# Performance work log

Hardware: AMD Instinct MI355X
Metric: run time of the kernel (lower is better)

## Reference

```python
import jax, jax.numpy as jnp
import numpy as np

B, N, D, H = 4, 512, 512, 8
DK = D // H
DIM_G = 64            # trignometric_embedding=True
WAVE_LEN = 1000.0


def box_relational_embedding(f_g):
    # f_g: [B, N, 4] = (x_min, x_max, y_min, y_max)
    x_min, x_max, y_min, y_max = jnp.split(f_g, 4, axis=-1)   # each [B, N, 1]
    cx = (x_min + x_max) * 0.5
    cy = (y_min + y_max) * 0.5
    w = x_max - x_min + 1.0
    h = y_max - y_min + 1.0
    # pairwise deltas: [B, N, 1] - [B, 1, N] -> [B, N, N]
    dx = jnp.log(jnp.clip(jnp.abs((cx - jnp.swapaxes(cx, 1, 2)) / w), 1e-3, None))
    dy = jnp.log(jnp.clip(jnp.abs((cy - jnp.swapaxes(cy, 1, 2)) / h), 1e-3, None))
    dw = jnp.log(w / jnp.swapaxes(w, 1, 2))
    dh = jnp.log(h / jnp.swapaxes(h, 1, 2))
    pos = jnp.stack([dx, dy, dw, dh], axis=-1)                # [B, N, N, 4]
    n_freq = DIM_G // 8                                       # 8
    feat_range = jnp.arange(n_freq, dtype=pos.dtype) / n_freq
    dim_mat = 1.0 / (WAVE_LEN ** feat_range)                  # [8]
    mul = (100.0 * pos)[..., None] * dim_mat                  # [B, N, N, 4, 8]
    mul = mul.reshape(B, N, N, 4 * n_freq)                    # [B, N, N, 32]
    return jnp.concatenate([jnp.sin(mul), jnp.cos(mul)], axis=-1)  # [B, N, N, 64]


def setup_inputs() -> dict:
    key = jax.random.key(0)
    ks = jax.random.split(key, 12)
    s = 0.02
    return {
        "input_query": jax.random.normal(ks[0], (B, N, D), jnp.float32),
        "input_key": jax.random.normal(ks[1], (B, N, D), jnp.float32),
        "input_value": jax.random.normal(ks[2], (B, N, D), jnp.float32),
        "input_box": jax.random.uniform(ks[3], (B, N, 4), jnp.float32),
        "mask": jnp.ones((B, N, N), jnp.int32),
        # 4 d_model->d_model linears (q, k, v, out); stored as [in, out]
        "Wq": jax.random.normal(ks[4], (D, D), jnp.float32) * s,
        "bq": jnp.zeros((D,), jnp.float32),
        "Wk": jax.random.normal(ks[5], (D, D), jnp.float32) * s,
        "bk": jnp.zeros((D,), jnp.float32),
        "Wv": jax.random.normal(ks[6], (D, D), jnp.float32) * s,
        "bv": jnp.zeros((D,), jnp.float32),
        "Wo": jax.random.normal(ks[7], (D, D), jnp.float32) * s,
        "bo": jnp.zeros((D,), jnp.float32),
        # the 8 per-head WGs (dim_g -> 1) stacked into a single [dim_g, H] matrix
        "Wg": jax.random.normal(ks[8], (DIM_G, H), jnp.float32) * s,
        "bg": jnp.zeros((H,), jnp.float32),
    }


def reference(input_query, input_key, input_value, input_box, mask,
              Wq, bq, Wk, bk, Wv, bv, Wo, bo, Wg, bg):
    # geometry embeddings -> per-head geometric weights
    geo_emb = box_relational_embedding(input_box)                 # [B, N, N, 64]
    geo_w = jax.nn.relu(jnp.einsum("bijg,gh->bhij", geo_emb, Wg)
                        + bg[None, :, None, None])                # [B, H, N, N]

    # q/k/v projections split into heads
    q = (input_query @ Wq + bq).reshape(B, N, H, DK)
    k = (input_key @ Wk + bk).reshape(B, N, H, DK)
    v = (input_value @ Wv + bv).reshape(B, N, H, DK)

    scores = jnp.einsum("bqhd,bkhd->bhqk", q, k) / np.sqrt(DK)    # [B, H, N, N]
    scores = jnp.where(mask[:, None, :, :] == 0, -1e9, scores)

    logits = jnp.log(jnp.clip(geo_w, 1e-6, None)) + scores
    attn = jax.nn.softmax(logits, axis=-1)                        # [B, H, N, N]

    out = jnp.einsum("bhqk,bkhd->bqhd", attn, v).reshape(B, N, D)
    return out @ Wo + bo                                          # [B, N, D]
```

## Files before the change

kernel.cpp:

```cpp
#include <hip/hip_runtime.h>
#include <hip/hip_bf16.h>

#define Bq 4
#define Nn 512
#define Dd 512
#define Hh 8
#define DKk 64

typedef __bf16 bf16x8 __attribute__((ext_vector_type(8)));
typedef float f32x4 __attribute__((ext_vector_type(4)));
typedef unsigned short u16x8 __attribute__((ext_vector_type(8)));

static __device__ __forceinline__ unsigned short f2bf(float f) {
    unsigned int u = __float_as_uint(f);
    return (unsigned short)((u + 0x7FFFu + ((u >> 16) & 1u)) >> 16);
}
static __device__ __forceinline__ unsigned short f2h(float f) {
    union { _Float16 h; unsigned short u; } cv;
    cv.h = (_Float16)f;
    return cv.u;
}
static __device__ __forceinline__ float h2f(unsigned short us) {
    union { _Float16 h; unsigned short u; } cv;
    cv.u = us;
    return (float)cv.h;
}

struct PreArgs {
    const float* A[3];
    const float* W[3];
    const float* bias[3];
    unsigned short* C[3];
    int ns[3], cs[3];
    float scale[3];
    const float* box;
    const int* mask;
    const float* Wg;
    const float* bg;
    unsigned short* lw;
};

__global__ __launch_bounds__(256) void pre_k(PreArgs pa)
{
    __shared__ __align__(16) char pool[10496];
    const int t = threadIdx.x;
    const int r_ = (int)(blockIdx.x % 19), g_ = (int)(blockIdx.x / 19);

    if (r_ < 16) {
        float (*WgS)[8] = (float(*)[8])pool;
        float* bgS = (float*)(pool + 2048);
        if (t < 128) ((float4*)&WgS[0][0])[t] = ((const float4*)pa.Wg)[t];
        if (t < 8) bgS[t] = pa.bg[t];
        __syncthreads();

        const int gb = g_ * 16 + r_;
        const size_t gid = (size_t)gb * 256 + t;
        const int j = (int)(gid & (Nn - 1));
        const int i = (int)((gid >> 9) & (Nn - 1));
        const int b = (int)(gid >> 18);

        const float4 bi = *(const float4*)(pa.box + ((size_t)b * Nn + i) * 4);
        const float4 bj = *(const float4*)(pa.box + ((size_t)b * Nn + j) * 4);
        const float cxi = (bi.x + bi.y) * 0.5f, cyi = (bi.z + bi.w) * 0.5f;
        const float wi = bi.y - bi.x + 1.0f, hi = bi.w - bi.z + 1.0f;
        const float cxj = (bj.x + bj.y) * 0.5f, cyj = (bj.z + bj.w) * 0.5f;
        const float wj = bj.y - bj.x + 1.0f, hj = bj.w - bj.z + 1.0f;

        const float pos0 = __logf(fmaxf(fabsf((cxi - cxj) / wi), 1e-3f));
        const float pos1 = __logf(fmaxf(fabsf((cyi - cyj) / hi), 1e-3f));
        const float pos2 = __logf(wi / wj);
        const float pos3 = __logf(hi / hj);

        const float dimr[8] = {1.0f, 0.421696503f, 0.177827941f, 0.0749894209f,
                               0.0316227766f, 0.0133352143f, 0.00562341325f, 0.00237137371f};

        float acc[8] = {0.f, 0.f, 0.f, 0.f, 0.f, 0.f, 0.f, 0.f};
#pragma unroll 1
        for (int p = 0; p < 4; ++p) {
            const float base = 100.0f * ((p == 0) ? pos0 : (p == 1) ? pos1 : (p == 2) ? pos2 : pos3);
            const int g0 = p << 3;
#pragma unroll
            for (int f = 0; f < 8; ++f) {
                float s, c;
                __sincosf(base * dimr[f], &s, &c);
                const int g = g0 + f;
                const float4 wa = *(const float4*)&WgS[g][0];
                const float4 wb = *(const float4*)&WgS[g][4];
                const float4 ca = *(const float4*)&WgS[g + 32][0];
                const float4 cb = *(const float4*)&WgS[g + 32][4];
                acc[0] = fmaf(s, wa.x, fmaf(c, ca.x, acc[0]));
                acc[1] = fmaf(s, wa.y, fmaf(c, ca.y, acc[1]));
                acc[2] = fmaf(s, wa.z, fmaf(c, ca.z, acc[2]));
                acc[3] = fmaf(s, wa.w, fmaf(c, ca.w, acc[3]));
                acc[4] = fmaf(s, wb.x, fmaf(c, cb.x, acc[4]));
                acc[5] = fmaf(s, wb.y, fmaf(c, cb.y, acc[5]));
                acc[6] = fmaf(s, wb.z, fmaf(c, cb.z, acc[6]));
                acc[7] = fmaf(s, wb.w, fmaf(c, cb.w, acc[7]));
            }
        }

        const int mk = pa.mask[gid];
        const size_t ob_ = (size_t)b * Hh * Nn * Nn + (size_t)i * Nn + j;
#pragma unroll
        for (int hh = 0; hh < 8; ++hh) {
            const float gw = acc[hh] + bgS[hh];
            const float lwv = (mk == 0) ? -60000.0f : __logf(fmaxf(gw, 1e-6f));
            pa.lw[ob_ + (size_t)hh * Nn * Nn] = f2h(lwv);
        }
    } else {
        unsigned short (*Alds)[40] = (unsigned short(*)[40])pool;
        unsigned short (*Blds)[40] = (unsigned short(*)[40])(pool + 5120);
        const int qid = g_ * 3 + (r_ - 16);
        const int z = qid % 3, tid = qid / 3;
        const int col0 = (tid & 7) << 6, row0 = (tid >> 3) << 6;
        const float* __restrict__ A = pa.A[z];
        const float* __restrict__ W = pa.W[z];

        const int l = t & 63, wq = t >> 6;
        const int lr = t >> 2, lc8 = (t & 3) << 3;
        const int bn = t & 63, bk8 = (t >> 6) << 3;
        const int lrow = l & 15, lgrp = l >> 4;

        f32x4 acc[4];
#pragma unroll
        for (int nf = 0; nf < 4; ++nf) acc[nf] = (f32x4){0.f, 0.f, 0.f, 0.f};

        for (int k0 = 0; k0 < Dd; k0 += 32) {
            const float* Ap = A + (size_t)(row0 + lr) * Dd + k0 + lc8;
            const float4 f1 = *(const float4*)Ap;
            const float4 f2 = *(const float4*)(Ap + 4);
            u16x8 a8;
            a8[0] = f2bf(f1.x); a8[1] = f2bf(f1.y); a8[2] = f2bf(f1.z); a8[3] = f2bf(f1.w);
            a8[4] = f2bf(f2.x); a8[5] = f2bf(f2.y); a8[6] = f2bf(f2.z); a8[7] = f2bf(f2.w);
            u16x8 b8;
#pragma unroll
            for (int jj = 0; jj < 8; ++jj)
                b8[jj] = f2bf(W[(size_t)(k0 + bk8 + jj) * Dd + col0 + bn]);
            __syncthreads();
            *(u16x8*)&Alds[lr][lc8] = a8;
            *(u16x8*)&Blds[bn][bk8] = b8;
            __syncthreads();
            const bf16x8 a = *(const bf16x8*)&Alds[wq * 16 + lrow][lgrp << 3];
#pragma unroll
            for (int nf = 0; nf < 4; ++nf) {
                const bf16x8 bfr = *(const bf16x8*)&Blds[nf * 16 + lrow][lgrp << 3];
                acc[nf] = __builtin_amdgcn_mfma_f32_16x16x32_bf16(a, bfr, acc[nf], 0, 0, 0);
            }
        }

        const float* bias = pa.bias[z];
        const float scl = pa.scale[z];
        const int ns = pa.ns[z], cs = pa.cs[z];
        const int rbase = row0 + wq * 16 + (lgrp << 2);
#pragma unroll
        for (int nf = 0; nf < 4; ++nf) {
            const int colg = col0 + nf * 16 + lrow;
            const float bv = bias[colg];
#pragma unroll
            for (int r = 0; r < 4; ++r) {
                const int rowg = rbase + r;
                const size_t addr = (size_t)(rowg >> 9) * ((size_t)Nn * Dd)
                                  + (size_t)(rowg & (Nn - 1)) * ns + (size_t)colg * cs;
                pa.C[z][addr] = f2bf((acc[nf][r] + bv) * scl);
            }
        }
    }
}

__global__ __launch_bounds__(256) void attn_k(
    const unsigned short* __restrict__ qb, const unsigned short* __restrict__ kb,
    const unsigned short* __restrict__ vt, const unsigned short* __restrict__ lwh,
    unsigned short* __restrict__ ob)
{
    __shared__ unsigned short Qlds[64][72];
    __shared__ unsigned short Klds[64][72];
    __shared__ unsigned short Vlds[64][72];
    __shared__ unsigned short Plds[4][16][72];
    __shared__ unsigned short LWs[64][72];

    const int t = threadIdx.x;
    const int l = t & 63, wq = t >> 6;
    const int bx = blockIdx.x;
    const int qt = bx & 7, h = (bx >> 3) & 7, b = bx >> 6;
    const int q0 = qt << 6;
    const int sr = t >> 3, sc8 = (t & 7) << 3;
    const int lrow = l & 15, lgrp = l >> 4;
    const int qr0 = t >> 3, c80 = (t & 7) << 3;
    const int qr1 = 32 + (t >> 3), c81 = c80;

    const size_t lwb = ((size_t)(b * Hh + h) * Nn + q0) * Nn;

#pragma unroll
    for (int it = 0; it < 2; ++it) {
        const int r = it * 32 + sr;
        *(u16x8*)&Qlds[r][sc8] =
            *(const u16x8*)(qb + (((size_t)b * Nn + q0 + r) * Hh + h) * DKk + sc8);
    }

    u16x8 kr[2], vr[2], lwr[2];
#pragma unroll
    for (int it = 0; it < 2; ++it) {
        const int r = it * 32 + sr;
        kr[it] = *(const u16x8*)(kb + (((size_t)b * Nn + r) * Hh + h) * DKk + sc8);
        vr[it] = *(const u16x8*)(vt + ((size_t)(b * Hh + h) * DKk + r) * Nn + sc8);
    }
    lwr[0] = *(const u16x8*)(lwh + lwb + (size_t)qr0 * Nn + c80);
    lwr[1] = *(const u16x8*)(lwh + lwb + (size_t)qr1 * Nn + c81);
#pragma unroll
    for (int it = 0; it < 2; ++it) {
        const int r = it * 32 + sr;
        *(u16x8*)&Klds[r][sc8] = kr[it];
        *(u16x8*)&Vlds[r][sc8] = vr[it];
    }
    *(u16x8*)&LWs[qr0][c80] = lwr[0];
    *(u16x8*)&LWs[qr1][c81] = lwr[1];
    __syncthreads();

    bf16x8 qa[2];
    qa[0] = *(const bf16x8*)&Qlds[wq * 16 + lrow][lgrp << 3];
    qa[1] = *(const bf16x8*)&Qlds[wq * 16 + lrow][32 + (lgrp << 3)];

    float m[4], lsum[4];
    f32x4 oacc[4];
#pragma unroll
    for (int r = 0; r < 4; ++r) { m[r] = -1e30f; lsum[r] = 0.f; }
#pragma unroll
    for (int fd = 0; fd < 4; ++fd) oacc[fd] = (f32x4){0.f, 0.f, 0.f, 0.f};

    for (int c = 0; c < 8; ++c) {
        if (c) __syncthreads();
        if (c < 7) {
            const int k1 = (c + 1) << 6;
#pragma unroll
            for (int it = 0; it < 2; ++it) {
                const int r = it * 32 + sr;
                kr[it] = *(const u16x8*)(kb + (((size_t)b * Nn + k1 + r) * Hh + h) * DKk + sc8);
                vr[it] = *(const u16x8*)(vt + ((size_t)(b * Hh + h) * DKk + r) * Nn + k1 + sc8);
            }
            lwr[0] = *(const u16x8*)(lwh + lwb + (size_t)qr0 * Nn + k1 + c80);
            lwr[1] = *(const u16x8*)(lwh + lwb + (size_t)qr1 * Nn + k1 + c81);
        }

        f32x4 sacc[4];
#pragma unroll
        for (int f = 0; f < 4; ++f) sacc[f] = (f32x4){0.f, 0.f, 0.f, 0.f};
#pragma unroll
        for (int ks = 0; ks < 2; ++ks)
#pragma unroll
            for (int f = 0; f < 4; ++f) {
                const bf16x8 kf = *(const bf16x8*)&Klds[f * 16 + lrow][(ks << 5) + (lgrp << 3)];
                sacc[f] = __builtin_amdgcn_mfma_f32_16x16x32_bf16(qa[ks], kf, sacc[f], 0, 0, 0);
            }

        float p[4][4], mx[4];
#pragma unroll
        for (int r = 0; r < 4; ++r) mx[r] = -1e30f;
#pragma unroll
        for (int f = 0; f < 4; ++f) {
#pragma unroll
            for (int r = 0; r < 4; ++r) {
                const float lg = sacc[f][r] + h2f(LWs[wq * 16 + lgrp * 4 + r][f * 16 + lrow]);
                p[f][r] = lg;
                mx[r] = fmaxf(mx[r], lg);
            }
        }
#pragma unroll
        for (int r = 0; r < 4; ++r) {
            float cm = mx[r];
            cm = fmaxf(cm, __shfl_xor(cm, 1));
            cm = fmaxf(cm, __shfl_xor(cm, 2));
            cm = fmaxf(cm, __shfl_xor(cm, 4));
            cm = fmaxf(cm, __shfl_xor(cm, 8));
            const float mn = fmaxf(m[r], cm);
            const float sc = __expf(m[r] - mn);
            m[r] = mn;
            float ps = 0.f;
#pragma unroll
            for (int f = 0; f < 4; ++f) {
                p[f][r] = __expf(p[f][r] - mn);
                ps += p[f][r];
            }
            ps += __shfl_xor(ps, 1);
            ps += __shfl_xor(ps, 2);
            ps += __shfl_xor(ps, 4);
            ps += __shfl_xor(ps, 8);
            lsum[r] = lsum[r] * sc + ps;
#pragma unroll
            for (int fd = 0; fd < 4; ++fd) oacc[fd][r] *= sc;
        }

#pragma unroll
        for (int f = 0; f < 4; ++f)
#pragma unroll
            for (int r = 0; r < 4; ++r)
                Plds[wq][lgrp * 4 + r][f * 16 + lrow] = f2bf(p[f][r]);

#pragma unroll
        for (int ks = 0; ks < 2; ++ks) {
            const bf16x8 pa = *(const bf16x8*)&Plds[wq][lrow][(ks << 5) + (lgrp << 3)];
#pragma unroll
            for (int fd = 0; fd < 4; ++fd) {
                const bf16x8 vf = *(const bf16x8*)&Vlds[fd * 16 + lrow][(ks << 5) + (lgrp << 3)];
                oacc[fd] = __builtin_amdgcn_mfma_f32_16x16x32_bf16(pa, vf, oacc[fd], 0, 0, 0);
            }
        }

        if (c < 7) {
            __syncthreads();
#pragma unroll
            for (int it = 0; it < 2; ++it) {
                const int r = it * 32 + sr;
                *(u16x8*)&Klds[r][sc8] = kr[it];
                *(u16x8*)&Vlds[r][sc8] = vr[it];
            }
            *(u16x8*)&LWs[qr0][c80] = lwr[0];
            *(u16x8*)&LWs[qr1][c81] = lwr[1];
        }
    }

#pragma unroll
    for (int r = 0; r < 4; ++r) {
        const float inv = 1.0f / lsum[r];
        const int qrow = q0 + wq * 16 + lgrp * 4 + r;
#pragma unroll
        for (int fd = 0; fd < 4; ++fd) {
            ob[(((size_t)b * Nn + qrow) * Hh + h) * DKk + fd * 16 + lrow] =
                f2bf(oacc[fd][r] * inv);
        }
    }
}

__global__ __launch_bounds__(256) void outproj_k(
    const unsigned short* __restrict__ A, const float* __restrict__ W,
    const float* __restrict__ bias, float* __restrict__ C)
{
    __shared__ unsigned short Alds[64][40];
    __shared__ unsigned short Blds[64][40];
    const int t = threadIdx.x;
    const int l = t & 63, wq = t >> 6;
    const int col0 = (int)(blockIdx.x) << 6, row0 = (int)(blockIdx.y) << 6;
    const int lr = t >> 2, lc8 = (t & 3) << 3;
    const int bn = t & 63, bk8 = (t >> 6) << 3;
    const int lrow = l & 15, lgrp = l >> 4;

    f32x4 acc[4];
#pragma unroll
    for (int nf = 0; nf < 4; ++nf) acc[nf] = (f32x4){0.f, 0.f, 0.f, 0.f};

    for (int k0 = 0; k0 < Dd; k0 += 32) {
        const u16x8 a8 = *(const u16x8*)(A + (size_t)(row0 + lr) * Dd + k0 + lc8);
        u16x8 b8;
#pragma unroll
        for (int jj = 0; jj < 8; ++jj)
            b8[jj] = f2bf(W[(size_t)(k0 + bk8 + jj) * Dd + col0 + bn]);
        __syncthreads();
        *(u16x8*)&Alds[lr][lc8] = a8;
        *(u16x8*)&Blds[bn][bk8] = b8;
        __syncthreads();
        const bf16x8 a = *(const bf16x8*)&Alds[wq * 16 + lrow][lgrp << 3];
#pragma unroll
        for (int nf = 0; nf < 4; ++nf) {
            const bf16x8 bfr = *(const bf16x8*)&Blds[nf * 16 + lrow][lgrp << 3];
            acc[nf] = __builtin_amdgcn_mfma_f32_16x16x32_bf16(a, bfr, acc[nf], 0, 0, 0);
        }
    }

    const int rbase = row0 + wq * 16 + (lgrp << 2);
#pragma unroll
    for (int nf = 0; nf < 4; ++nf) {
        const int colg = col0 + nf * 16 + lrow;
        const float bv = bias[colg];
#pragma unroll
        for (int r = 0; r < 4; ++r)
            C[(size_t)(rbase + r) * Dd + colg] = acc[nf][r] + bv;
    }
}

extern "C" void kernel_launch(void* const* d_in, const int* in_sizes, int n_in,
                              void* d_out, int out_size, void* d_ws, size_t ws_size,
                              hipStream_t stream)
{
    (void)in_sizes; (void)n_in; (void)out_size; (void)ws_size;

    const float* q_in = (const float*)d_in[0];
    const float* k_in = (const float*)d_in[1];
    const float* v_in = (const float*)d_in[2];
    const float* box  = (const float*)d_in[3];
    const int*   mask = (const int*)d_in[4];
    const float* Wq = (const float*)d_in[5];
    const float* bq = (const float*)d_in[6];
    const float* Wk = (const float*)d_in[7];
    const float* bk = (const float*)d_in[8];
    const float* Wv = (const float*)d_in[9];
    const float* bv = (const float*)d_in[10];
    const float* Wo = (const float*)d_in[11];
    const float* bo = (const float*)d_in[12];
    const float* Wg = (const float*)d_in[13];
    const float* bg = (const float*)d_in[14];
    float* out = (float*)d_out;

    char* ws = (char*)d_ws;
    unsigned short* qb  = (unsigned short*)(ws);
    unsigned short* kb  = (unsigned short*)(ws + (2u << 20));
    unsigned short* vt  = (unsigned short*)(ws + (4u << 20));
    unsigned short* ob  = (unsigned short*)(ws + (6u << 20));
    unsigned short* lwh = (unsigned short*)(ws + (8u << 20));

    PreArgs pa;
    pa.A[0] = q_in; pa.A[1] = k_in; pa.A[2] = v_in;
    pa.W[0] = Wq;   pa.W[1] = Wk;   pa.W[2] = Wv;
    pa.bias[0] = bq; pa.bias[1] = bk; pa.bias[2] = bv;
    pa.C[0] = qb; pa.C[1] = kb; pa.C[2] = vt;
    pa.ns[0] = Dd; pa.ns[1] = Dd; pa.ns[2] = 1;
    pa.cs[0] = 1;  pa.cs[1] = 1;  pa.cs[2] = Nn;
    pa.scale[0] = 0.125f; pa.scale[1] = 1.0f; pa.scale[2] = 1.0f;
    pa.box = box; pa.mask = mask; pa.Wg = Wg; pa.bg = bg; pa.lw = lwh;
    pre_k<<<dim3(4864), 256, 0, stream>>>(pa);

    attn_k<<<dim3(Bq * Hh * (Nn / 64)), 256, 0, stream>>>(qb, kb, vt, lwh, ob);

    outproj_k<<<dim3(8, 32), 256, 0, stream>>>(ob, Wo, bo, out);
}
```

Before: 76.92 us.

## Compute geometry embedding projection with fp16 MFMA, one feature group per lane

The geometry bias path no longer has each thread evaluate all 32 sin/cos pairs and 64x8 scalar FMAs. Each lane now computes one of the four position components and its 8 frequencies, and the 64->8 Wg projection runs as two 16x16x32 fp16 MFMAs with half the N columns zero-padded. This cuts transcendental and FMA work per pair roughly fourfold and changes the grid to 64 geometry blocks plus 3 GEMM blocks per group. The cost is fp16 rounding of sin/cos and weights, wasted MFMA columns, and mask and Wg loads repeated per lane. LDS row padding also changes from 40 to 44 in the projection tiles.

```diff
diff --git a/kernel.cpp b/kernel.cpp
--- a/kernel.cpp
+++ b/kernel.cpp
@@ -8,6 +8,7 @@
 #define DKk 64
 
 typedef __bf16 bf16x8 __attribute__((ext_vector_type(8)));
+typedef _Float16 f16x8 __attribute__((ext_vector_type(8)));
 typedef float f32x4 __attribute__((ext_vector_type(4)));
 typedef unsigned short u16x8 __attribute__((ext_vector_type(8)));
 
@@ -42,84 +43,75 @@
 
 __global__ __launch_bounds__(256) void pre_k(PreArgs pa)
 {
-    __shared__ __align__(16) char pool[10496];
+    __shared__ __align__(16) unsigned short ABlds[2][64][44];
     const int t = threadIdx.x;
-    const int r_ = (int)(blockIdx.x % 19), g_ = (int)(blockIdx.x / 19);
-
-    if (r_ < 16) {
-        float (*WgS)[8] = (float(*)[8])pool;
-        float* bgS = (float*)(pool + 2048);
-        if (t < 128) ((float4*)&WgS[0][0])[t] = ((const float4*)pa.Wg)[t];
-        if (t < 8) bgS[t] = pa.bg[t];
-        __syncthreads();
-
-        const int gb = g_ * 16 + r_;
-        const size_t gid = (size_t)gb * 256 + t;
-        const int j = (int)(gid & (Nn - 1));
-        const int i = (int)((gid >> 9) & (Nn - 1));
-        const int b = (int)(gid >> 18);
-
-        const float4 bi = *(const float4*)(pa.box + ((size_t)b * Nn + i) * 4);
+    const int r_ = (int)(blockIdx.x % 67), g_ = (int)(blockIdx.x / 67);
+    const int l = t & 63, wq = t >> 6;
+    const int lrow = l & 15, lgrp = l >> 4;
+
+    if (r_ < 64) {
+        const int geo = g_ * 64 + r_;
+        const int j0 = (geo & 7) << 6;
+        const int ib = geo >> 3;
+        const int b = ib >> 9, i = ib & (Nn - 1);
+        const int jw = j0 + wq * 16;
+        const int j = jw + lrow;
+
+        const float4 bi = *(const float4*)(pa.box + (size_t)ib * 4);
         const float4 bj = *(const float4*)(pa.box + ((size_t)b * Nn + j) * 4);
-        const float cxi = (bi.x + bi.y) * 0.5f, cyi = (bi.z + bi.w) * 0.5f;
-        const float wi = bi.y - bi.x + 1.0f, hi = bi.w - bi.z + 1.0f;
-        const float cxj = (bj.x + bj.y) * 0.5f, cyj = (bj.z + bj.w) * 0.5f;
-        const float wj = bj.y - bj.x + 1.0f, hj = bj.w - bj.z + 1.0f;
-
-        const float pos0 = __logf(fmaxf(fabsf((cxi - cxj) / wi), 1e-3f));
-        const float pos1 = __logf(fmaxf(fabsf((cyi - cyj) / hi), 1e-3f));
-        const float pos2 = __logf(wi / wj);
-        const float pos3 = __logf(hi / hj);
+
+        float u0, u1, u2, u3;
+        if (lgrp & 1) { u0 = bi.z; u1 = bi.w; u2 = bj.z; u3 = bj.w; }
+        else          { u0 = bi.x; u1 = bi.y; u2 = bj.x; u3 = bj.y; }
+        const float di = u1 - u0 + 1.0f, dj = u3 - u2 + 1.0f;
+        float val;
+        if (lgrp < 2) val = fmaxf(fabsf((u0 + u1) * 0.5f - (u2 + u3) * 0.5f) / di, 1e-3f);
+        else          val = di / dj;
+        const float base = 100.0f * __logf(val);
 
         const float dimr[8] = {1.0f, 0.421696503f, 0.177827941f, 0.0749894209f,
                                0.0316227766f, 0.0133352143f, 0.00562341325f, 0.00237137371f};
 
-        float acc[8] = {0.f, 0.f, 0.f, 0.f, 0.f, 0.f, 0.f, 0.f};
-#pragma unroll 1
-        for (int p = 0; p < 4; ++p) {
-            const float base = 100.0f * ((p == 0) ? pos0 : (p == 1) ? pos1 : (p == 2) ? pos2 : pos3);
-            const int g0 = p << 3;
-#pragma unroll
-            for (int f = 0; f < 8; ++f) {
-                float s, c;
-                __sincosf(base * dimr[f], &s, &c);
-                const int g = g0 + f;
-                const float4 wa = *(const float4*)&WgS[g][0];
-                const float4 wb = *(const float4*)&WgS[g][4];
-                const float4 ca = *(const float4*)&WgS[g + 32][0];
-                const float4 cb = *(const float4*)&WgS[g + 32][4];
-                acc[0] = fmaf(s, wa.x, fmaf(c, ca.x, acc[0]));
-                acc[1] = fmaf(s, wa.y, fmaf(c, ca.y, acc[1]));
-                acc[2] = fmaf(s, wa.z, fmaf(c, ca.z, acc[2]));
-                acc[3] = fmaf(s, wa.w, fmaf(c, ca.w, acc[3]));
-                acc[4] = fmaf(s, wb.x, fmaf(c, cb.x, acc[4]));
-                acc[5] = fmaf(s, wb.y, fmaf(c, cb.y, acc[5]));
-                acc[6] = fmaf(s, wb.z, fmaf(c, cb.z, acc[6]));
-                acc[7] = fmaf(s, wb.w, fmaf(c, cb.w, acc[7]));
-            }
-        }
-
-        const int mk = pa.mask[gid];
-        const size_t ob_ = (size_t)b * Hh * Nn * Nn + (size_t)i * Nn + j;
-#pragma unroll
-        for (int hh = 0; hh < 8; ++hh) {
-            const float gw = acc[hh] + bgS[hh];
+        f16x8 a0, a1;
+#pragma unroll
+        for (int m = 0; m < 8; ++m) {
+            float s, c;
+            __sincosf(base * dimr[m], &s, &c);
+            a0[m] = (_Float16)s;
+            a1[m] = (_Float16)c;
+        }
+        f16x8 w0, w1;
+#pragma unroll
+        for (int m = 0; m < 8; ++m) {
+            const int g = lgrp * 8 + m;
+            w0[m] = (lrow < 8) ? (_Float16)pa.Wg[(size_t)g * Hh + lrow] : (_Float16)0.0f;
+            w1[m] = (lrow < 8) ? (_Float16)pa.Wg[(size_t)(32 + g) * Hh + lrow] : (_Float16)0.0f;
+        }
+        f32x4 cfr = (f32x4){0.f, 0.f, 0.f, 0.f};
+        cfr = __builtin_amdgcn_mfma_f32_16x16x32_f16(a0, w0, cfr, 0, 0, 0);
+        cfr = __builtin_amdgcn_mfma_f32_16x16x32_f16(a1, w1, cfr, 0, 0, 0);
+
+        const float bgv = (lrow < 8) ? pa.bg[lrow] : 0.0f;
+        const size_t mbase = (size_t)ib * Nn + jw;
+        const size_t obase = (((size_t)b * Hh + lrow) * Nn + i) * Nn + jw;
+#pragma unroll
+        for (int r = 0; r < 4; ++r) {
+            const int row = lgrp * 4 + r;
+            const int mk = pa.mask[mbase + row];
+            const float gw = cfr[r] + bgv;
             const float lwv = (mk == 0) ? -60000.0f : __logf(fmaxf(gw, 1e-6f));
-            pa.lw[ob_ + (size_t)hh * Nn * Nn] = f2h(lwv);
+            if (lrow < 8)
+                pa.lw[obase + row] = f2h(lwv);
         }
     } else {
-        unsigned short (*Alds)[40] = (unsigned short(*)[40])pool;
-        unsigned short (*Blds)[40] = (unsigned short(*)[40])(pool + 5120);
-        const int qid = g_ * 3 + (r_ - 16);
+        const int qid = g_ * 3 + (r_ - 64);
         const int z = qid % 3, tid = qid / 3;
         const int col0 = (tid & 7) << 6, row0 = (tid >> 3) << 6;
         const float* __restrict__ A = pa.A[z];
         const float* __restrict__ W = pa.W[z];
 
-        const int l = t & 63, wq = t >> 6;
         const int lr = t >> 2, lc8 = (t & 3) << 3;
         const int bn = t & 63, bk8 = (t >> 6) << 3;
-        const int lrow = l & 15, lgrp = l >> 4;
 
         f32x4 acc[4];
 #pragma unroll
@@ -137,13 +129,13 @@
             for (int jj = 0; jj < 8; ++jj)
                 b8[jj] = f2bf(W[(size_t)(k0 + bk8 + jj) * Dd + col0 + bn]);
             __syncthreads();
-            *(u16x8*)&Alds[lr][lc8] = a8;
-            *(u16x8*)&Blds[bn][bk8] = b8;
+            *(u16x8*)&ABlds[0][lr][lc8] = a8;
+            *(u16x8*)&ABlds[1][bn][bk8] = b8;
             __syncthreads();
-            const bf16x8 a = *(const bf16x8*)&Alds[wq * 16 + lrow][lgrp << 3];
+            const bf16x8 a = *(const bf16x8*)&ABlds[0][wq * 16 + lrow][lgrp << 3];
 #pragma unroll
             for (int nf = 0; nf < 4; ++nf) {
-                const bf16x8 bfr = *(const bf16x8*)&Blds[nf * 16 + lrow][lgrp << 3];
+                const bf16x8 bfr = *(const bf16x8*)&ABlds[1][nf * 16 + lrow][lgrp << 3];
                 acc[nf] = __builtin_amdgcn_mfma_f32_16x16x32_bf16(a, bfr, acc[nf], 0, 0, 0);
             }
         }
@@ -297,11 +289,11 @@
 
 #pragma unroll
         for (int ks = 0; ks < 2; ++ks) {
-            const bf16x8 pa = *(const bf16x8*)&Plds[wq][lrow][(ks << 5) + (lgrp << 3)];
+            const bf16x8 pafr = *(const bf16x8*)&Plds[wq][lrow][(ks << 5) + (lgrp << 3)];
 #pragma unroll
             for (int fd = 0; fd < 4; ++fd) {
                 const bf16x8 vf = *(const bf16x8*)&Vlds[fd * 16 + lrow][(ks << 5) + (lgrp << 3)];
-                oacc[fd] = __builtin_amdgcn_mfma_f32_16x16x32_bf16(pa, vf, oacc[fd], 0, 0, 0);
+                oacc[fd] = __builtin_amdgcn_mfma_f32_16x16x32_bf16(pafr, vf, oacc[fd], 0, 0, 0);
             }
         }
 
@@ -334,8 +326,8 @@
     const unsigned short* __restrict__ A, const float* __restrict__ W,
     const float* __restrict__ bias, float* __restrict__ C)
 {
-    __shared__ unsigned short Alds[64][40];
-    __shared__ unsigned short Blds[64][40];
+    __shared__ unsigned short Alds[64][44];
+    __shared__ unsigned short Blds[64][44];
     const int t = threadIdx.x;
     const int l = t & 63, wq = t >> 6;
     const int col0 = (int)(blockIdx.x) << 6, row0 = (int)(blockIdx.y) << 6;
@@ -415,7 +407,7 @@
     pa.cs[0] = 1;  pa.cs[1] = 1;  pa.cs[2] = Nn;
     pa.scale[0] = 0.125f; pa.scale[1] = 1.0f; pa.scale[2] = 1.0f;
     pa.box = box; pa.mask = mask; pa.Wg = Wg; pa.bg = bg; pa.lw = lwh;
-    pre_k<<<dim3(4864), 256, 0, stream>>>(pa);
+    pre_k<<<dim3(67 * 256), 256, 0, stream>>>(pa);
 
     attn_k<<<dim3(Bq * Hh * (Nn / 64)), 256, 0, stream>>>(qb, kb, vt, lwh, ob);
 
```

Result: slower. 103.9 us (+35.0%).

## Compute geometry-embedding projection with fp16 MFMA through LDS staging

Applied to the files above, without the earlier changes.

The geometric weight projection (64-dim sin/cos embedding times the 64x8 Wg matrix) now stages each thread's embedding row as fp16 in shared memory and runs 16x16x32 f16 MFMAs per wave, replacing the scalar FMA accumulation. Results go back to LDS so each thread can read its own 8 head values. This grows shared memory per block from about 10KB to about 48KB, which may lower occupancy, and adds fp16 rounding to the embedding. GEMM LDS row padding also changes from 40 to 44.

```diff
diff --git a/kernel.cpp b/kernel.cpp
--- a/kernel.cpp
+++ b/kernel.cpp
@@ -8,6 +8,7 @@
 #define DKk 64
 
 typedef __bf16 bf16x8 __attribute__((ext_vector_type(8)));
+typedef _Float16 f16x8 __attribute__((ext_vector_type(8)));
 typedef float f32x4 __attribute__((ext_vector_type(4)));
 typedef unsigned short u16x8 __attribute__((ext_vector_type(8)));
 
@@ -42,15 +43,23 @@
 
 __global__ __launch_bounds__(256) void pre_k(PreArgs pa)
 {
-    __shared__ __align__(16) char pool[10496];
+    __shared__ __align__(16) char pool[48384];
     const int t = threadIdx.x;
     const int r_ = (int)(blockIdx.x % 19), g_ = (int)(blockIdx.x / 19);
+    const int l = t & 63, wq = t >> 6;
+    const int lrow = l & 15, lgrp = l >> 4;
 
     if (r_ < 16) {
-        float (*WgS)[8] = (float(*)[8])pool;
-        float* bgS = (float*)(pool + 2048);
-        if (t < 128) ((float4*)&WgS[0][0])[t] = ((const float4*)pa.Wg)[t];
-        if (t < 8) bgS[t] = pa.bg[t];
+        unsigned short* embS = (unsigned short*)pool;
+        float* gwS = (float*)(pool + 36864);
+        unsigned short* wgS = (unsigned short*)(pool + 46080);
+
+#pragma unroll
+        for (int it = 0; it < 2; ++it) {
+            const int idx = it * 256 + t;
+            const int hh = idx >> 6, kk = idx & 63;
+            wgS[hh * 72 + kk] = f2h(pa.Wg[(size_t)kk * Hh + hh]);
+        }
         __syncthreads();
 
         const int gb = g_ * 16 + r_;
@@ -74,52 +83,62 @@
         const float dimr[8] = {1.0f, 0.421696503f, 0.177827941f, 0.0749894209f,
                                0.0316227766f, 0.0133352143f, 0.00562341325f, 0.00237137371f};
 
-        float acc[8] = {0.f, 0.f, 0.f, 0.f, 0.f, 0.f, 0.f, 0.f};
+        unsigned short* erow = embS + (size_t)t * 72;
 #pragma unroll 1
         for (int p = 0; p < 4; ++p) {
             const float base = 100.0f * ((p == 0) ? pos0 : (p == 1) ? pos1 : (p == 2) ? pos2 : pos3);
-            const int g0 = p << 3;
+            f16x8 s8, c8;
 #pragma unroll
             for (int f = 0; f < 8; ++f) {
                 float s, c;
                 __sincosf(base * dimr[f], &s, &c);
-                const int g = g0 + f;
-                const float4 wa = *(const float4*)&WgS[g][0];
-                const float4 wb = *(const float4*)&WgS[g][4];
-                const float4 ca = *(const float4*)&WgS[g + 32][0];
-                const float4 cb = *(const float4*)&WgS[g + 32][4];
-                acc[0] = fmaf(s, wa.x, fmaf(c, ca.x, acc[0]));
-                acc[1] = fmaf(s, wa.y, fmaf(c, ca.y, acc[1]));
-                acc[2] = fmaf(s, wa.z, fmaf(c, ca.z, acc[2]));
-                acc[3] = fmaf(s, wa.w, fmaf(c, ca.w, acc[3]));
-                acc[4] = fmaf(s, wb.x, fmaf(c, cb.x, acc[4]));
-                acc[5] = fmaf(s, wb.y, fmaf(c, cb.y, acc[5]));
-                acc[6] = fmaf(s, wb.z, fmaf(c, cb.z, acc[6]));
-                acc[7] = fmaf(s, wb.w, fmaf(c, cb.w, acc[7]));
-            }
+                s8[f] = (_Float16)s;
+                c8[f] = (_Float16)c;
+            }
+            *(f16x8*)&erow[p * 8] = s8;
+            *(f16x8*)&erow[32 + p * 8] = c8;
+        }
+
+        const f16x8 bf0 = *(const f16x8*)&wgS[lrow * 72 + lgrp * 8];
+        const f16x8 bf1 = *(const f16x8*)&wgS[lrow * 72 + 32 + lgrp * 8];
+        f32x4 cfr[4];
+#pragma unroll
+        for (int g = 0; g < 4; ++g) {
+            cfr[g] = (f32x4){0.f, 0.f, 0.f, 0.f};
+            const unsigned short* arow = embS + (size_t)(wq * 64 + g * 16 + lrow) * 72;
+            const f16x8 a0 = *(const f16x8*)&arow[lgrp * 8];
+            cfr[g] = __builtin_amdgcn_mfma_f32_16x16x32_f16(a0, bf0, cfr[g], 0, 0, 0);
+            const f16x8 a1 = *(const f16x8*)&arow[32 + lgrp * 8];
+            cfr[g] = __builtin_amdgcn_mfma_f32_16x16x32_f16(a1, bf1, cfr[g], 0, 0, 0);
+        }
+
+        if (lrow < 8) {
+#pragma unroll
+            for (int g = 0; g < 4; ++g)
+#pragma unroll
+                for (int r = 0; r < 4; ++r)
+                    gwS[(size_t)(wq * 64 + g * 16 + lgrp * 4 + r) * 9 + lrow] = cfr[g][r];
         }
 
         const int mk = pa.mask[gid];
         const size_t ob_ = (size_t)b * Hh * Nn * Nn + (size_t)i * Nn + j;
+        const float* grow = gwS + (size_t)t * 9;
 #pragma unroll
         for (int hh = 0; hh < 8; ++hh) {
-            const float gw = acc[hh] + bgS[hh];
+            const float gw = grow[hh] + pa.bg[hh];
             const float lwv = (mk == 0) ? -60000.0f : __logf(fmaxf(gw, 1e-6f));
             pa.lw[ob_ + (size_t)hh * Nn * Nn] = f2h(lwv);
         }
     } else {
-        unsigned short (*Alds)[40] = (unsigned short(*)[40])pool;
-        unsigned short (*Blds)[40] = (unsigned short(*)[40])(pool + 5120);
+        unsigned short (*ABlds)[64][44] = (unsigned short(*)[64][44])pool;
         const int qid = g_ * 3 + (r_ - 16);
         const int z = qid % 3, tid = qid / 3;
         const int col0 = (tid & 7) << 6, row0 = (tid >> 3) << 6;
         const float* __restrict__ A = pa.A[z];
         const float* __restrict__ W = pa.W[z];
 
-        const int l = t & 63, wq = t >> 6;
         const int lr = t >> 2, lc8 = (t & 3) << 3;
         const int bn = t & 63, bk8 = (t >> 6) << 3;
-        const int lrow = l & 15, lgrp = l >> 4;
 
         f32x4 acc[4];
 #pragma unroll
@@ -137,13 +156,13 @@
             for (int jj = 0; jj < 8; ++jj)
                 b8[jj] = f2bf(W[(size_t)(k0 + bk8 + jj) * Dd + col0 + bn]);
             __syncthreads();
-            *(u16x8*)&Alds[lr][lc8] = a8;
-            *(u16x8*)&Blds[bn][bk8] = b8;
+            *(u16x8*)&ABlds[0][lr][lc8] = a8;
+            *(u16x8*)&ABlds[1][bn][bk8] = b8;
             __syncthreads();
-            const bf16x8 a = *(const bf16x8*)&Alds[wq * 16 + lrow][lgrp << 3];
+            const bf16x8 a = *(const bf16x8*)&ABlds[0][wq * 16 + lrow][lgrp << 3];
 #pragma unroll
             for (int nf = 0; nf < 4; ++nf) {
-                const bf16x8 bfr = *(const bf16x8*)&Blds[nf * 16 + lrow][lgrp << 3];
+                const bf16x8 bfr = *(const bf16x8*)&ABlds[1][nf * 16 + lrow][lgrp << 3];
                 acc[nf] = __builtin_amdgcn_mfma_f32_16x16x32_bf16(a, bfr, acc[nf], 0, 0, 0);
             }
         }
@@ -297,11 +316,11 @@
 
 #pragma unroll
         for (int ks = 0; ks < 2; ++ks) {
-            const bf16x8 pa = *(const bf16x8*)&Plds[wq][lrow][(ks << 5) + (lgrp << 3)];
+            const bf16x8 pafr = *(const bf16x8*)&Plds[wq][lrow][(ks << 5) + (lgrp << 3)];
 #pragma unroll
             for (int fd = 0; fd < 4; ++fd) {
                 const bf16x8 vf = *(const bf16x8*)&Vlds[fd * 16 + lrow][(ks << 5) + (lgrp << 3)];
-                oacc[fd] = __builtin_amdgcn_mfma_f32_16x16x32_bf16(pa, vf, oacc[fd], 0, 0, 0);
+                oacc[fd] = __builtin_amdgcn_mfma_f32_16x16x32_bf16(pafr, vf, oacc[fd], 0, 0, 0);
             }
         }
 
@@ -334,8 +353,8 @@
     const unsigned short* __restrict__ A, const float* __restrict__ W,
     const float* __restrict__ bias, float* __restrict__ C)
 {
-    __shared__ unsigned short Alds[64][40];
-    __shared__ unsigned short Blds[64][40];
+    __shared__ unsigned short Alds[64][44];
+    __shared__ unsigned short Blds[64][44];
     const int t = threadIdx.x;
     const int l = t & 63, wq = t >> 6;
     const int col0 = (int)(blockIdx.x) << 6, row0 = (int)(blockIdx.y) << 6;
```

Result: slower. 112.6 us (+46.3%).
